# Performance work log

Hardware: AMD Instinct MI355X
Metric: run time of the kernel (lower is better)

Reference implementation:

```python
import math
import jax, jax.numpy as jnp
import numpy as np

FACIL_RATE = 2.0
FIRE_THRESH = 0.85
MAX_GATE = 8.0
EPS = 1e-12  # F.normalize eps

B, T, D = 8, 4096, 2048


def _gelu(x):
    # tanh-approx GELU, exactly as in the torch module
    c = math.sqrt(2.0 / math.pi)
    return 0.5 * x * (1.0 + jnp.tanh(c * (x + 0.044715 * x * x * x)))


def _l2norm(v, axis=-1):
    n = jnp.sqrt(jnp.sum(v * v, axis=axis, keepdims=True))
    return v / jnp.maximum(n, EPS)


def setup_inputs() -> dict:
    key = jax.random.key(0)
    k1, k2 = jax.random.split(key)
    x = jax.random.normal(k1, (B, T, D), dtype=jnp.float32)
    pos_buf = jax.random.normal(k2, (T, D), dtype=jnp.float32)
    pos_facil = jnp.ones((T,), dtype=jnp.float32)
    log_k_pos = jnp.asarray(math.log(0.5), dtype=jnp.float32)
    return {"x": x, "log_k_pos": log_k_pos, "pos_buf": pos_buf, "pos_facil": pos_facil}


def reference(x, log_k_pos, pos_buf, pos_facil):
    # steady-state (pass1 complete) path of GELU275.forward
    k_pos = jnp.clip(jnp.exp(log_k_pos), 0.01, 5.0)
    y = _gelu(x)                                   # [B,T,D]
    # everything below the gelu except the final gate multiply runs under
    # no_grad / on y.detach() in torch -> stop_gradient here
    y_det = jax.lax.stop_gradient(y)
    pos_buf_n = _l2norm(jax.lax.stop_gradient(pos_buf))          # [T,D]
    y_n = _l2norm(y_det)                                          # [B,T,D]
    sim = jnp.einsum("btd,td->bt", y_n, pos_buf_n)               # cosine sim [B,T]
    fire_mask = jnp.mean(sim, axis=0) > FIRE_THRESH              # [T]
    pf = jax.lax.stop_gradient(pos_facil)
    facil_t = jnp.where(fire_mask, jnp.minimum(pf * FACIL_RATE, 16.0), pf)  # [T]
    gate = jnp.minimum(1.0 + k_pos * (facil_t[None, :] - 1.0) * sim, MAX_GATE)  # [B,T]
    return y * gate[:, :, None]
```

## Files before the change

### kernel.cpp

```cpp
#include <hip/hip_runtime.h>
#include <math.h>

#define BB 8
#define TT 4096
#define DD 2048
#define THREADS 256
#define NWAVES (THREADS / 64)

typedef float v4f __attribute__((ext_vector_type(4)));

__device__ __forceinline__ float fast_tanh(float a) {
    float e = __expf(2.0f * a);
    return 1.0f - 2.0f / (e + 1.0f);
}

__device__ __forceinline__ float gelu_tanh(float x) {
    const float c = 0.7978845608028654f;
    float inner = c * (x + 0.044715f * x * x * x);
    return 0.5f * x * (1.0f + fast_tanh(inner));
}

__device__ __forceinline__ void gelu4_dot(v4f& v, const v4f& p,
                                          float& d, float& n) {
    v.x = gelu_tanh(v.x); v.y = gelu_tanh(v.y);
    v.z = gelu_tanh(v.z); v.w = gelu_tanh(v.w);
    d += v.x * p.x + v.y * p.y + v.z * p.z + v.w * p.w;
    n += v.x * v.x + v.y * v.y + v.z * v.z + v.w * v.w;
}

__global__ __launch_bounds__(THREADS, 4) void gelu275_fused(
    const float* __restrict__ x,
    const float* __restrict__ log_k_pos,
    const float* __restrict__ pos_buf,
    const float* __restrict__ pos_facil,
    float* __restrict__ out)
{
    const int t    = blockIdx.x;
    const int tid  = threadIdx.x;
    const int lane = tid & 63;
    const int wave = tid >> 6;

    __shared__ float red[NWAVES][17];

    const size_t col = (size_t)tid * 8;

    v4f xa[BB], xb[BB];
#pragma unroll
    for (int b = 0; b < BB; ++b) {
        const float* px = x + ((size_t)b * TT + t) * DD + col;
        xa[b] = *reinterpret_cast<const v4f*>(px);
        xb[b] = *reinterpret_cast<const v4f*>(px + 4);
    }
    const float* pp = pos_buf + (size_t)t * DD + col;
    const v4f pa = *reinterpret_cast<const v4f*>(pp);
    const v4f pb = *reinterpret_cast<const v4f*>(pp + 4);

    float pn2 = pa.x*pa.x + pa.y*pa.y + pa.z*pa.z + pa.w*pa.w
              + pb.x*pb.x + pb.y*pb.y + pb.z*pb.z + pb.w*pb.w;

    float dotp[BB], yn2[BB];
#pragma unroll
    for (int b = 0; b < BB; ++b) {
        float d = 0.0f, n = 0.0f;
        gelu4_dot(xa[b], pa, d, n);
        gelu4_dot(xb[b], pb, d, n);
        dotp[b] = d;
        yn2[b]  = n;
    }

#pragma unroll
    for (int off = 32; off; off >>= 1) {
        pn2 += __shfl_xor(pn2, off);
#pragma unroll
        for (int b = 0; b < BB; ++b) {
            dotp[b] += __shfl_xor(dotp[b], off);
            yn2[b]  += __shfl_xor(yn2[b],  off);
        }
    }
    if (lane == 0) {
        red[wave][0] = pn2;
#pragma unroll
        for (int b = 0; b < BB; ++b) {
            red[wave][1 + b] = dotp[b];
            red[wave][9 + b] = yn2[b];
        }
    }
    __syncthreads();

    const int myb = lane & 7;
    float P = 0.0f, Dt = 0.0f, Yn = 0.0f;
#pragma unroll
    for (int w = 0; w < NWAVES; ++w) {
        P  += red[w][0];
        Dt += red[w][1 + myb];
        Yn += red[w][9 + myb];
    }
    const float kp = fminf(fmaxf(__expf(log_k_pos[0]), 0.01f), 5.0f);
    const float pn = fmaxf(sqrtf(P),  1e-12f);
    const float yn = fmaxf(sqrtf(Yn), 1e-12f);
    const float sim = Dt / (yn * pn);

    float simsum = sim;
    simsum += __shfl_xor(simsum, 1);
    simsum += __shfl_xor(simsum, 2);
    simsum += __shfl_xor(simsum, 4);

    const bool  fire  = (simsum * (1.0f / BB)) > 0.85f;
    const float pf    = pos_facil[t];
    const float facil = fire ? fminf(pf * 2.0f, 16.0f) : pf;
    const float myg   = fminf(1.0f + kp * (facil - 1.0f) * sim, 8.0f);

#pragma unroll
    for (int b = 0; b < BB; ++b) {
        const float g = __shfl(myg, b, 8);
        float* po = out + ((size_t)b * TT + t) * DD + col;
        v4f o0, o1;
        o0.x = xa[b].x * g; o0.y = xa[b].y * g;
        o0.z = xa[b].z * g; o0.w = xa[b].w * g;
        o1.x = xb[b].x * g; o1.y = xb[b].y * g;
        o1.z = xb[b].z * g; o1.w = xb[b].w * g;
        __builtin_nontemporal_store(o0, reinterpret_cast<v4f*>(po));
        __builtin_nontemporal_store(o1, reinterpret_cast<v4f*>(po + 4));
    }
}

extern "C" void kernel_launch(void* const* d_in, const int* in_sizes, int n_in,
                              void* d_out, int out_size, void* d_ws, size_t ws_size,
                              hipStream_t stream) {
    const float* x          = (const float*)d_in[0];
    const float* log_k_pos  = (const float*)d_in[1];
    const float* pos_buf    = (const float*)d_in[2];
    const float* pos_facil  = (const float*)d_in[3];
    float* out              = (float*)d_out;

    dim3 grid(TT);
    dim3 block(THREADS);
    gelu275_fused<<<grid, block, 0, stream>>>(x, log_k_pos, pos_buf, pos_facil, out);
}
```

Measured before the change: 130.7 us.

## Assign one wave per batch row with 512-thread blocks and wave-local reductions

Reorganizes the per-token block so that each of 8 waves owns one batch row, reading the full 2048-wide row in coalesced float4 chunks. Each wave reduces its own dot product and norm with shuffles instead of the earlier multi-batch shuffle trees and cross-wave shared-memory sums. Every wave now reloads the pos_buf row, which adds redundant load traffic. Output stores switch from nontemporal to ordinary stores, which may change cache behavior on a memory-bound kernel.

```diff
diff --git a/kernel.cpp b/kernel.cpp
--- a/kernel.cpp
+++ b/kernel.cpp
@@ -4,8 +4,8 @@
 #define BB 8
 #define TT 4096
 #define DD 2048
-#define THREADS 256
-#define NWAVES (THREADS / 64)
+#define THREADS 512
+#define CHUNKS 8
 
 typedef float v4f __attribute__((ext_vector_type(4)));
 
@@ -20,15 +20,7 @@
     return 0.5f * x * (1.0f + fast_tanh(inner));
 }
 
-__device__ __forceinline__ void gelu4_dot(v4f& v, const v4f& p,
-                                          float& d, float& n) {
-    v.x = gelu_tanh(v.x); v.y = gelu_tanh(v.y);
-    v.z = gelu_tanh(v.z); v.w = gelu_tanh(v.w);
-    d += v.x * p.x + v.y * p.y + v.z * p.z + v.w * p.w;
-    n += v.x * v.x + v.y * v.y + v.z * v.z + v.w * v.w;
-}
-
-__global__ __launch_bounds__(THREADS, 4) void gelu275_fused(
+__global__ __launch_bounds__(THREADS) void gelu275_fused(
     const float* __restrict__ x,
     const float* __restrict__ log_k_pos,
     const float* __restrict__ pos_buf,
@@ -40,87 +32,70 @@
     const int lane = tid & 63;
     const int wave = tid >> 6;
 
-    __shared__ float red[NWAVES][17];
+    __shared__ float s_dot[BB];
+    __shared__ float s_yn2[BB];
+    __shared__ float s_pn2;
 
-    const size_t col = (size_t)tid * 8;
+    const float* xrow = x       + ((size_t)wave * TT + t) * DD;
+    const float* prow = pos_buf + (size_t)t * DD;
+    const int    base = lane * 4;
 
-    v4f xa[BB], xb[BB];
+    v4f xv[CHUNKS], pv[CHUNKS];
 #pragma unroll
-    for (int b = 0; b < BB; ++b) {
-        const float* px = x + ((size_t)b * TT + t) * DD + col;
-        xa[b] = *reinterpret_cast<const v4f*>(px);
-        xb[b] = *reinterpret_cast<const v4f*>(px + 4);
-    }
-    const float* pp = pos_buf + (size_t)t * DD + col;
-    const v4f pa = *reinterpret_cast<const v4f*>(pp);
-    const v4f pb = *reinterpret_cast<const v4f*>(pp + 4);
+    for (int c = 0; c < CHUNKS; ++c)
+        xv[c] = *reinterpret_cast<const v4f*>(xrow + c * 256 + base);
+#pragma unroll
+    for (int c = 0; c < CHUNKS; ++c)
+        pv[c] = *reinterpret_cast<const v4f*>(prow + c * 256 + base);
 
-    float pn2 = pa.x*pa.x + pa.y*pa.y + pa.z*pa.z + pa.w*pa.w
-              + pb.x*pb.x + pb.y*pb.y + pb.z*pb.z + pb.w*pb.w;
-
-    float dotp[BB], yn2[BB];
+    float dot = 0.0f, yn2 = 0.0f, pn2 = 0.0f;
 #pragma unroll
-    for (int b = 0; b < BB; ++b) {
-        float d = 0.0f, n = 0.0f;
-        gelu4_dot(xa[b], pa, d, n);
-        gelu4_dot(xb[b], pb, d, n);
-        dotp[b] = d;
-        yn2[b]  = n;
+    for (int c = 0; c < CHUNKS; ++c) {
+        v4f& v = xv[c];
+        const v4f& p = pv[c];
+        v.x = gelu_tanh(v.x); v.y = gelu_tanh(v.y);
+        v.z = gelu_tanh(v.z); v.w = gelu_tanh(v.w);
+        dot += v.x * p.x + v.y * p.y + v.z * p.z + v.w * p.w;
+        yn2 += v.x * v.x + v.y * v.y + v.z * v.z + v.w * v.w;
+        pn2 += p.x * p.x + p.y * p.y + p.z * p.z + p.w * p.w;
     }
 
 #pragma unroll
     for (int off = 32; off; off >>= 1) {
+        dot += __shfl_xor(dot, off);
+        yn2 += __shfl_xor(yn2, off);
         pn2 += __shfl_xor(pn2, off);
-#pragma unroll
-        for (int b = 0; b < BB; ++b) {
-            dotp[b] += __shfl_xor(dotp[b], off);
-            yn2[b]  += __shfl_xor(yn2[b],  off);
-        }
     }
     if (lane == 0) {
-        red[wave][0] = pn2;
-#pragma unroll
-        for (int b = 0; b < BB; ++b) {
-            red[wave][1 + b] = dotp[b];
-            red[wave][9 + b] = yn2[b];
-        }
+        s_dot[wave] = dot;
+        s_yn2[wave] = yn2;
+        if (wave == 0) s_pn2 = pn2;
     }
     __syncthreads();
 
-    const int myb = lane & 7;
-    float P = 0.0f, Dt = 0.0f, Yn = 0.0f;
+    const float kp = fminf(fmaxf(__expf(log_k_pos[0]), 0.01f), 5.0f);
+    const float pn = fmaxf(sqrtf(s_pn2), 1e-12f);
+
+    float simsum = 0.0f;
+    float simw   = 0.0f;
 #pragma unroll
-    for (int w = 0; w < NWAVES; ++w) {
-        P  += red[w][0];
-        Dt += red[w][1 + myb];
-        Yn += red[w][9 + myb];
+    for (int b = 0; b < BB; ++b) {
+        const float s = s_dot[b] / (fmaxf(sqrtf(s_yn2[b]), 1e-12f) * pn);
+        simsum += s;
+        if (b == wave) simw = s;
     }
-    const float kp = fminf(fmaxf(__expf(log_k_pos[0]), 0.01f), 5.0f);
-    const float pn = fmaxf(sqrtf(P),  1e-12f);
-    const float yn = fmaxf(sqrtf(Yn), 1e-12f);
-    const float sim = Dt / (yn * pn);
-
-    float simsum = sim;
-    simsum += __shfl_xor(simsum, 1);
-    simsum += __shfl_xor(simsum, 2);
-    simsum += __shfl_xor(simsum, 4);
-
     const bool  fire  = (simsum * (1.0f / BB)) > 0.85f;
     const float pf    = pos_facil[t];
     const float facil = fire ? fminf(pf * 2.0f, 16.0f) : pf;
-    const float myg   = fminf(1.0f + kp * (facil - 1.0f) * sim, 8.0f);
+    const float g     = fminf(1.0f + kp * (facil - 1.0f) * simw, 8.0f);
 
+    float* orow = out + ((size_t)wave * TT + t) * DD;
 #pragma unroll
-    for (int b = 0; b < BB; ++b) {
-        const float g = __shfl(myg, b, 8);
-        float* po = out + ((size_t)b * TT + t) * DD + col;
-        v4f o0, o1;
-        o0.x = xa[b].x * g; o0.y = xa[b].y * g;
-        o0.z = xa[b].z * g; o0.w = xa[b].w * g;
-        o1.x = xb[b].x * g; o1.y = xb[b].y * g;
-        o1.z = xb[b].z * g; o1.w = xb[b].w * g;
-        __builtin_nontemporal_store(o0, reinterpret_cast<v4f*>(po));
-        __builtin_nontemporal_store(o1, reinterpret_cast<v4f*>(po + 4));
+    for (int c = 0; c < CHUNKS; ++c) {
+        v4f o;
+        o.x = xv[c].x * g; o.y = xv[c].y * g;
+        o.z = xv[c].z * g; o.w = xv[c].w * g;
+        *reinterpret_cast<v4f*>(orow + c * 256 + base) = o;
     }
 }
 
```

Result: faster. 126.6 us (-3.1%).
